# Kernel optimization log

Measured on AMD Instinct MI355X. Metric: run time of the kernel, lower is better.

## Reference

```python
import jax, jax.numpy as jnp
import numpy as np

N = 100000
IN_DIM = 128
OUT_DIM = 128
HEADS = 4
C = OUT_DIM // HEADS  # per-head channels = 32
E = 1600000
EPS = 1e-5
NEG_SLOPE = 0.2


def setup_inputs() -> dict:
    key = jax.random.key(0)
    ks = jax.random.split(key, 10)
    prev = jax.random.normal(ks[0], (N, OUT_DIM), dtype=jnp.float32)
    x = jax.random.normal(ks[1], (N, IN_DIM), dtype=jnp.float32)
    edge_index = jax.random.randint(ks[2], (2, E), 0, N, dtype=jnp.int32)
    # GATConv parameters (glorot-ish scale)
    W = jax.random.normal(ks[3], (IN_DIM, HEADS * C), dtype=jnp.float32) * (1.0 / np.sqrt(IN_DIM))
    att_src = jax.random.normal(ks[4], (HEADS, C), dtype=jnp.float32) * (1.0 / np.sqrt(C))
    att_dst = jax.random.normal(ks[5], (HEADS, C), dtype=jnp.float32) * (1.0 / np.sqrt(C))
    bias = jnp.zeros((HEADS * C,), dtype=jnp.float32)
    # BatchNorm1d affine params
    gamma = jnp.ones((OUT_DIM,), dtype=jnp.float32)
    beta = jnp.zeros((OUT_DIM,), dtype=jnp.float32)
    return {"prev": prev, "x": x, "edge_index": edge_index, "W": W,
            "att_src": att_src, "att_dst": att_dst, "bias": bias,
            "gamma": gamma, "beta": beta}


def reference(prev, x, edge_index, W, att_src, att_dst, bias, gamma, beta):
    # --- GATConv (PyG defaults: add_self_loops=True, concat=True, neg_slope=0.2) ---
    n = x.shape[0]
    # add self loops
    loops = jnp.arange(n, dtype=edge_index.dtype)
    src = jnp.concatenate([edge_index[0], loops])  # [E+N] message source j
    dst = jnp.concatenate([edge_index[1], loops])  # [E+N] message target i

    h = (x @ W).reshape(n, HEADS, C)               # [N,H,C]
    a_src = jnp.einsum('nhc,hc->nh', h, att_src)   # [N,H]
    a_dst = jnp.einsum('nhc,hc->nh', h, att_dst)   # [N,H]

    alpha = a_src[src] + a_dst[dst]                # [E',H]
    alpha = jax.nn.leaky_relu(alpha, NEG_SLOPE)
    # segment softmax over incoming edges of each dst node
    amax = jax.ops.segment_max(alpha, dst, num_segments=n)       # [N,H]
    alpha = jnp.exp(alpha - amax[dst])
    asum = jax.ops.segment_sum(alpha, dst, num_segments=n)       # [N,H]
    alpha = alpha / asum[dst]

    msg = h[src] * alpha[:, :, None]                              # [E',H,C]
    out = jax.ops.segment_sum(msg, dst, num_segments=n)          # [N,H,C]
    out = out.reshape(n, HEADS * C) + bias                       # concat heads + bias

    # --- residual + BatchNorm1d (training-mode batch stats) + activation ---
    y = prev + out
    mean = jnp.mean(y, axis=0)
    var = jnp.mean(jnp.square(y - mean), axis=0)  # biased variance (torch BN)
    y = gamma * (y - mean) * jax.lax.rsqrt(var + EPS) + beta
    return jax.nn.relu(y)
```

## Files before the change

### kernel.cpp

```cpp
#include <hip/hip_runtime.h>
#include <math.h>

#define DIM 128
#define NEG 0.2f
#define EPS 1e-5f
#define LOG2E 1.4426950408889634f

#if __has_builtin(__builtin_amdgcn_exp2f)
#define EXP2(x) __builtin_amdgcn_exp2f(x)
#else
#define EXP2(x) exp2f(x)
#endif

typedef __attribute__((ext_vector_type(8))) short short8v;
typedef __attribute__((ext_vector_type(4))) float f32x4;

static __device__ __forceinline__ float leaky(float a) { return a > 0.f ? a : NEG * a; }
static __device__ __forceinline__ float bf2f(unsigned short u) {
    return __uint_as_float(((unsigned int)u) << 16);
}
static __device__ __forceinline__ unsigned short f2bf(float f) {
    unsigned int u = __float_as_uint(f);
    unsigned int r = (u + 0x7fffu + ((u >> 16) & 1u)) >> 16;
    return (unsigned short)r;
}

__global__ __launch_bounds__(256) void k_gemm(const float* __restrict__ x,
                                              const float* __restrict__ W,
                                              const float* __restrict__ att_s,
                                              const float* __restrict__ att_d,
                                              unsigned int* __restrict__ hpk,
                                              float* __restrict__ asrc,
                                              float* __restrict__ adst, int n) {
    __shared__ __align__(16) unsigned short xs[16][136];
    const int tid = threadIdx.x;
    const int w = tid >> 6;
    const int lane = tid & 63;
    const int lm = lane & 15;
    const int lk = lane >> 4;
    short8v bfrag[2][4];
#pragma unroll
    for (int ct = 0; ct < 2; ++ct) {
        int c = w * 32 + ct * 16 + lm;
#pragma unroll
        for (int q = 0; q < 4; ++q) {
            short8v f;
#pragma unroll
            for (int j = 0; j < 8; ++j) {
                int k = q * 32 + lk * 8 + j;
                f[j] = (short)f2bf(W[k * DIM + c]);
            }
            bfrag[ct][q] = f;
        }
    }
    const float asv0 = att_s[w * 32 + lm] * LOG2E;
    const float asv1 = att_s[w * 32 + 16 + lm] * LOG2E;
    const float adv0 = att_d[w * 32 + lm] * LOG2E;
    const float adv1 = att_d[w * 32 + 16 + lm] * LOG2E;

    const int nchunk = (n + 15) >> 4;
    for (int chunk = blockIdx.x; chunk < nchunk; chunk += gridDim.x) {
        const int r0 = chunk * 16;
        {
            int row = tid >> 4;
            int c8 = (tid & 15) * 8;
            int rg = min(r0 + row, n - 1);
            const float4* xp = (const float4*)(x + (size_t)rg * DIM + c8);
            float4 v0 = xp[0], v1 = xp[1];
            short8v t;
            t[0] = (short)f2bf(v0.x); t[1] = (short)f2bf(v0.y);
            t[2] = (short)f2bf(v0.z); t[3] = (short)f2bf(v0.w);
            t[4] = (short)f2bf(v1.x); t[5] = (short)f2bf(v1.y);
            t[6] = (short)f2bf(v1.z); t[7] = (short)f2bf(v1.w);
            *(short8v*)(&xs[row][c8]) = t;
        }
        __syncthreads();
        f32x4 acc0 = {0.f, 0.f, 0.f, 0.f}, acc1 = {0.f, 0.f, 0.f, 0.f};
#pragma unroll
        for (int q = 0; q < 4; ++q) {
            short8v a = *(const short8v*)(&xs[lm][q * 32 + lk * 8]);
            acc0 = __builtin_amdgcn_mfma_f32_16x16x32_bf16(a, bfrag[0][q], acc0, 0, 0, 0);
            acc1 = __builtin_amdgcn_mfma_f32_16x16x32_bf16(a, bfrag[1][q], acc1, 0, 0, 0);
        }
        __syncthreads();
        float ps[4], qs[4];
#pragma unroll
        for (int j = 0; j < 4; ++j) {
            ps[j] = acc0[j] * asv0 + acc1[j] * asv1;
            qs[j] = acc0[j] * adv0 + acc1[j] * adv1;
        }
#pragma unroll
        for (int m = 1; m < 16; m <<= 1) {
#pragma unroll
            for (int j = 0; j < 4; ++j) {
                ps[j] += __shfl_xor(ps[j], m);
                qs[j] += __shfl_xor(qs[j], m);
            }
        }
#pragma unroll
        for (int j = 0; j < 4; ++j) {
            int r = r0 + 4 * lk + j;
            if (r < n) {
                hpk[(size_t)r * 64 + 16 * w + lm] =
                    (unsigned int)f2bf(acc0[j]) | ((unsigned int)f2bf(acc1[j]) << 16);
                if (lm == 0) {
                    asrc[r * 4 + w] = ps[j];
                    adst[r * 4 + w] = qs[j];
                }
            }
        }
    }
}

__global__ void k_init(int* __restrict__ deg, float* __restrict__ stats, int n) {
    int t = blockIdx.x * blockDim.x + threadIdx.x;
    if (t < n) deg[t] = 1;
    if (t < 256) stats[t] = 0.f;
}

__global__ __launch_bounds__(256) void k_hist(const int* __restrict__ dst,
                                              int* __restrict__ deg, int E, int n) {
    const int g = blockIdx.x & 7;
    const int gb = blockIdx.x >> 3;
    const int nblk = gridDim.x >> 3;
    const int wsz = (n + 7) >> 3;
    const int lo = g * wsz;
    const int hi = min(lo + wsz, n);
    const int step = nblk * 256;
    for (int t = gb * 256 + threadIdx.x; t < E; t += step) {
        int d = dst[t];
        if (d >= lo && d < hi) atomicAdd(&deg[d], 1);
    }
}

__global__ __launch_bounds__(256) void k_scan_part(const int* __restrict__ deg,
                                                   int* __restrict__ bsum, int n) {
    int idx = blockIdx.x * 1024 + threadIdx.x * 4;
    int4 v = {0, 0, 0, 0};
    if (idx + 3 < n) v = *(const int4*)(deg + idx);
    else {
        if (idx + 0 < n) v.x = deg[idx + 0];
        if (idx + 1 < n) v.y = deg[idx + 1];
        if (idx + 2 < n) v.z = deg[idx + 2];
    }
    int s = v.x + v.y + v.z + v.w;
#pragma unroll
    for (int m = 1; m < 64; m <<= 1) s += __shfl_xor(s, m);
    __shared__ int ws[4];
    if ((threadIdx.x & 63) == 0) ws[threadIdx.x >> 6] = s;
    __syncthreads();
    if (threadIdx.x == 0) bsum[blockIdx.x] = ws[0] + ws[1] + ws[2] + ws[3];
}

__global__ __launch_bounds__(256) void k_scan_tops(int* __restrict__ bsum, int B) {
    __shared__ int lds[256];
    int t = threadIdx.x;
    int v = (t < B) ? bsum[t] : 0;
    lds[t] = v;
    __syncthreads();
    int acc = v;
    for (int ofs = 1; ofs < 256; ofs <<= 1) {
        int u = (t >= ofs) ? lds[t - ofs] : 0;
        __syncthreads();
        acc += u;
        lds[t] = acc;
        __syncthreads();
    }
    if (t < B) bsum[t] = acc - v;
}

__global__ __launch_bounds__(256) void k_scan_add(const int* __restrict__ deg,
                                                  const int* __restrict__ bsum,
                                                  int* __restrict__ row_start,
                                                  int* __restrict__ cursor, int n, int total) {
    int t = threadIdx.x;
    int idx = blockIdx.x * 1024 + t * 4;
    int4 v = {0, 0, 0, 0};
    if (idx + 3 < n) v = *(const int4*)(deg + idx);
    else {
        if (idx + 0 < n) v.x = deg[idx + 0];
        if (idx + 1 < n) v.y = deg[idx + 1];
        if (idx + 2 < n) v.z = deg[idx + 2];
    }
    int s = v.x + v.y + v.z + v.w;
    __shared__ int lds[256];
    lds[t] = s;
    __syncthreads();
    int acc = s;
    for (int ofs = 1; ofs < 256; ofs <<= 1) {
        int u = (t >= ofs) ? lds[t - ofs] : 0;
        __syncthreads();
        acc += u;
        lds[t] = acc;
        __syncthreads();
    }
    int excl = bsum[blockIdx.x] + acc - s;
    int4 rs;
    rs.x = excl;
    rs.y = rs.x + v.x;
    rs.z = rs.y + v.y;
    rs.w = rs.z + v.z;
    if (idx + 3 < n) {
        *(int4*)(row_start + idx) = rs;
        *(int4*)(cursor + idx) = rs;
    } else {
        if (idx + 0 < n) { row_start[idx + 0] = rs.x; cursor[idx + 0] = rs.x; }
        if (idx + 1 < n) { row_start[idx + 1] = rs.y; cursor[idx + 1] = rs.y; }
        if (idx + 2 < n) { row_start[idx + 2] = rs.z; cursor[idx + 2] = rs.z; }
    }
    if (blockIdx.x == 0 && t == 0) row_start[n] = total;
}

__global__ __launch_bounds__(256) void k_scatter(const int* __restrict__ src,
                                                 const int* __restrict__ dst,
                                                 const float4* __restrict__ asrc4,
                                                 const float4* __restrict__ adst4,
                                                 int* __restrict__ cursor,
                                                 int* __restrict__ csr,
                                                 uint2* __restrict__ pw,
                                                 int E, int n) {
    const int g = blockIdx.x & 7;
    const int gb = blockIdx.x >> 3;
    const int nblk = gridDim.x >> 3;
    const int wsz = (n + 7) >> 3;
    const int lo = g * wsz;
    const int hi = min(lo + wsz, n);
    const int total = E + n;
    const int step = nblk * 256;
    for (int t = gb * 256 + threadIdx.x; t < total; t += step) {
        int d = (t < E) ? dst[t] : (t - E);
        if (d >= lo && d < hi) {
            int sv = (t < E) ? src[t] : d;
            float4 a = asrc4[sv];
            float4 b = adst4[d];
            float p0 = EXP2(leaky(a.x + b.x));
            float p1 = EXP2(leaky(a.y + b.y));
            float p2 = EXP2(leaky(a.z + b.z));
            float p3 = EXP2(leaky(a.w + b.w));
            int slot = atomicAdd(&cursor[d], 1);
            csr[slot] = sv;
            uint2 o;
            o.x = (unsigned int)f2bf(p0) | ((unsigned int)f2bf(p1) << 16);
            o.y = (unsigned int)f2bf(p2) | ((unsigned int)f2bf(p3) << 16);
            pw[slot] = o;
        }
    }
}

__global__ __launch_bounds__(256) void k_agg(const unsigned int* __restrict__ hw,
                                             const unsigned short* __restrict__ pwh,
                                             const int* __restrict__ row_start,
                                             const int* __restrict__ csr,
                                             const float* __restrict__ prev,
                                             const float* __restrict__ bias,
                                             float* __restrict__ ypre,
                                             float* __restrict__ stats, int n) {
    const int lane = threadIdx.x & 63;
    const int hd = lane >> 4;
    const int ch = 32 * hd + (lane & 15);
    int wave = blockIdx.x * 4 + (threadIdx.x >> 6);
    int nw = gridDim.x * 4;
    const float bb0 = bias[ch], bb1 = bias[ch + 16];
    float bsum0 = 0.f, bsq0 = 0.f, bsum1 = 0.f, bsq1 = 0.f;
    for (int i0 = wave; i0 < n; i0 += nw) {
        int i = __builtin_amdgcn_readfirstlane(i0);
        int e0 = row_start[i], e1 = row_start[i + 1];
        float s = 0.f, acc0 = 0.f, acc1 = 0.f;
        for (int e = e0; e < e1; e += 16) {
            int j[16];
            float p[16];
            unsigned int hp[16];
#pragma unroll
            for (int r = 0; r < 16; ++r) {
                int ec = min(e + r, e1 - 1);
                j[r] = csr[ec];
                p[r] = bf2f(pwh[ec * 4 + hd]);
            }
#pragma unroll
            for (int r = 0; r < 16; ++r) hp[r] = hw[(size_t)j[r] * 64 + lane];
#pragma unroll
            for (int r = 0; r < 16; ++r) {
                float pp = (e + r < e1) ? p[r] : 0.f;
                s += pp;
                acc0 = fmaf(pp, __uint_as_float(hp[r] << 16), acc0);
                acc1 = fmaf(pp, __uint_as_float(hp[r] & 0xffff0000u), acc1);
            }
        }
        float rs = 1.0f / s;
        size_t base = (size_t)i * DIM;
        float o0 = fmaf(acc0, rs, bb0 + prev[base + ch]);
        float o1 = fmaf(acc1, rs, bb1 + prev[base + ch + 16]);
        ypre[base + ch] = o0;
        ypre[base + ch + 16] = o1;
        bsum0 += o0; bsq0 = fmaf(o0, o0, bsq0);
        bsum1 += o1; bsq1 = fmaf(o1, o1, bsq1);
    }
    __shared__ float red[4][256];
    red[0][threadIdx.x] = bsum0;
    red[1][threadIdx.x] = bsq0;
    red[2][threadIdx.x] = bsum1;
    red[3][threadIdx.x] = bsq1;
    __syncthreads();
    if (threadIdx.x < 64) {
        int t = threadIdx.x;
        int c = 32 * (t >> 4) + (t & 15);
        float v0 = red[0][t] + red[0][t + 64] + red[0][t + 128] + red[0][t + 192];
        float v1 = red[1][t] + red[1][t + 64] + red[1][t + 128] + red[1][t + 192];
        float v2 = red[2][t] + red[2][t + 64] + red[2][t + 128] + red[2][t + 192];
        float v3 = red[3][t] + red[3][t + 64] + red[3][t + 128] + red[3][t + 192];
        atomicAdd(&stats[c], v0);
        atomicAdd(&stats[c + 16], v2);
        atomicAdd(&stats[128 + c], v1);
        atomicAdd(&stats[128 + c + 16], v3);
    }
}

__global__ void k_bnfin(const float* __restrict__ stats, const float* __restrict__ gamma,
                        const float* __restrict__ beta, float* __restrict__ AB, int n) {
    int c = threadIdx.x;
    float fn = (float)n;
    float mean = stats[c] / fn;
    float var = stats[128 + c] / fn - mean * mean;
    float a = gamma[c] * rsqrtf(var + EPS);
    AB[c] = a;
    AB[128 + c] = beta[c] - mean * a;
}

__global__ __launch_bounds__(256) void k_final(float* __restrict__ y,
                                               const float* __restrict__ AB, int total4) {
    int t0 = blockIdx.x * blockDim.x + threadIdx.x;
    int stride = gridDim.x * blockDim.x;
    for (int t = t0; t < total4; t += stride) {
        float4 v = ((float4*)y)[t];
        int c0 = (t * 4) & 127;
        v.x = fmaf(v.x, AB[c0 + 0], AB[128 + c0 + 0]);
        v.y = fmaf(v.y, AB[c0 + 1], AB[128 + c0 + 1]);
        v.z = fmaf(v.z, AB[c0 + 2], AB[128 + c0 + 2]);
        v.w = fmaf(v.w, AB[c0 + 3], AB[128 + c0 + 3]);
        v.x = v.x > 0.f ? v.x : 0.f;
        v.y = v.y > 0.f ? v.y : 0.f;
        v.z = v.z > 0.f ? v.z : 0.f;
        v.w = v.w > 0.f ? v.w : 0.f;
        ((float4*)y)[t] = v;
    }
}

extern "C" void kernel_launch(void* const* d_in, const int* in_sizes, int n_in,
                              void* d_out, int out_size, void* d_ws, size_t ws_size,
                              hipStream_t stream) {
    const float* prev  = (const float*)d_in[0];
    const float* x     = (const float*)d_in[1];
    const int*   ei    = (const int*)d_in[2];
    const float* W     = (const float*)d_in[3];
    const float* att_s = (const float*)d_in[4];
    const float* att_d = (const float*)d_in[5];
    const float* bias  = (const float*)d_in[6];
    const float* gamma = (const float*)d_in[7];
    const float* beta  = (const float*)d_in[8];
    const int n = in_sizes[0] / DIM;
    const int E = in_sizes[2] / 2;
    const int* src = ei;
    const int* dst = ei + E;

    char* p = (char*)d_ws;
    auto alloc = [&](size_t bytes) {
        void* q = (void*)p;
        p += (bytes + 255) & ~(size_t)255;
        return q;
    };
    unsigned int* hpk = (unsigned int*)alloc((size_t)n * 64 * 4);
    float* asrc      = (float*)alloc((size_t)n * 4 * 4);
    float* adst      = (float*)alloc((size_t)n * 4 * 4);
    int*   deg       = (int*)alloc((size_t)(n + 1) * 4);
    int*   row_start = (int*)alloc((size_t)(n + 1) * 4);
    int*   cursor    = (int*)alloc((size_t)(n + 1) * 4);
    int*   csr       = (int*)alloc((size_t)(E + n + 16) * 4);
    uint2* pw        = (uint2*)alloc((size_t)(E + n + 16) * 8);
    int*   bsum      = (int*)alloc(1024 * 4);
    float* stats     = (float*)alloc(256 * 4);
    float* AB        = (float*)alloc(256 * 4);
    float* yout      = (float*)d_out;

    int B = (n + 1023) / 1024;
    k_init<<<dim3((n + 255) / 256), dim3(256), 0, stream>>>(deg, stats, n);
    k_gemm<<<dim3(1024), dim3(256), 0, stream>>>(x, W, att_s, att_d, hpk, asrc, adst, n);
    k_hist<<<dim3(2048), dim3(256), 0, stream>>>(dst, deg, E, n);
    k_scan_part<<<dim3(B), dim3(256), 0, stream>>>(deg, bsum, n);
    k_scan_tops<<<dim3(1), dim3(256), 0, stream>>>(bsum, B);
    k_scan_add<<<dim3(B), dim3(256), 0, stream>>>(deg, bsum, row_start, cursor, n, E + n);
    k_scatter<<<dim3(2048), dim3(256), 0, stream>>>(src, dst, (const float4*)asrc,
                                                    (const float4*)adst, cursor, csr, pw, E, n);
    k_agg<<<dim3(2048), dim3(256), 0, stream>>>(hpk, (const unsigned short*)pw, row_start,
                                                csr, prev, bias, yout, stats, n);
    k_bnfin<<<dim3(1), dim3(128), 0, stream>>>(stats, gamma, beta, AB, n);
    int total4 = n * DIM / 4;
    k_final<<<dim3(2048), dim3(256), 0, stream>>>(yout, AB, total4);
}
```

Measured before the change: 312.2 us.

## Store pre-BN output as packed bf16 and remap agg waves to node ranges

The aggregation kernel now writes its pre-normalization output as packed bf16 pairs into a workspace buffer, and a new final kernel reads it, applies the BN affine transform and ReLU, and writes fp32. The aim is to cut the bytes of the intermediate write and read. Agg waves are also regrouped so that groups of blocks (blockIdx & 7) cover contiguous node ranges, likely to improve cache locality across XCDs. The packed path is used only when the workspace is large enough. It adds bf16 rounding of the pre-BN values, which is an accuracy risk.

Result: faster. 298.2 us (-4.5%).

```diff
diff --git a/kernel.cpp b/kernel.cpp
--- a/kernel.cpp
+++ b/kernel.cpp
@@ -247,6 +247,7 @@
     }
 }
 
+template <bool PACKED>
 __global__ __launch_bounds__(256) void k_agg(const unsigned int* __restrict__ hw,
                                              const unsigned short* __restrict__ pwh,
                                              const int* __restrict__ row_start,
@@ -254,15 +255,22 @@
                                              const float* __restrict__ prev,
                                              const float* __restrict__ bias,
                                              float* __restrict__ ypre,
+                                             unsigned int* __restrict__ ypb,
                                              float* __restrict__ stats, int n) {
     const int lane = threadIdx.x & 63;
     const int hd = lane >> 4;
     const int ch = 32 * hd + (lane & 15);
-    int wave = blockIdx.x * 4 + (threadIdx.x >> 6);
-    int nw = gridDim.x * 4;
+    const int g = blockIdx.x & 7;
+    const int gb = blockIdx.x >> 3;
+    const int nblk = gridDim.x >> 3;
+    const int wsz = (n + 7) >> 3;
+    const int lo = g * wsz;
+    const int hi = min(lo + wsz, n);
+    const int wig = gb * 4 + (threadIdx.x >> 6);
+    const int nwg = nblk * 4;
     const float bb0 = bias[ch], bb1 = bias[ch + 16];
     float bsum0 = 0.f, bsq0 = 0.f, bsum1 = 0.f, bsq1 = 0.f;
-    for (int i0 = wave; i0 < n; i0 += nw) {
+    for (int i0 = lo + wig; i0 < hi; i0 += nwg) {
         int i = __builtin_amdgcn_readfirstlane(i0);
         int e0 = row_start[i], e1 = row_start[i + 1];
         float s = 0.f, acc0 = 0.f, acc1 = 0.f;
@@ -290,8 +298,13 @@
         size_t base = (size_t)i * DIM;
         float o0 = fmaf(acc0, rs, bb0 + prev[base + ch]);
         float o1 = fmaf(acc1, rs, bb1 + prev[base + ch + 16]);
-        ypre[base + ch] = o0;
-        ypre[base + ch + 16] = o1;
+        if (PACKED) {
+            ypb[(size_t)i * 64 + lane] =
+                (unsigned int)f2bf(o0) | ((unsigned int)f2bf(o1) << 16);
+        } else {
+            ypre[base + ch] = o0;
+            ypre[base + ch + 16] = o1;
+        }
         bsum0 += o0; bsq0 = fmaf(o0, o0, bsq0);
         bsum1 += o1; bsq1 = fmaf(o1, o1, bsq1);
     }
@@ -326,6 +339,25 @@
     AB[128 + c] = beta[c] - mean * a;
 }
 
+__global__ __launch_bounds__(256) void k_final_pk(const unsigned int* __restrict__ ypb,
+                                                  const float* __restrict__ AB,
+                                                  float* __restrict__ yout, int totalw) {
+    int t0 = blockIdx.x * blockDim.x + threadIdx.x;
+    int stride = gridDim.x * blockDim.x;
+    for (int t = t0; t < totalw; t += stride) {
+        unsigned int wv = ypb[t];
+        int u = t & 63;
+        int row = t >> 6;
+        int c = 32 * (u >> 4) + (u & 15);
+        float o0 = bf2f((unsigned short)(wv & 0xffffu));
+        float o1 = bf2f((unsigned short)(wv >> 16));
+        float r0 = fmaf(o0, AB[c], AB[128 + c]);
+        float r1 = fmaf(o1, AB[c + 16], AB[128 + c + 16]);
+        yout[(size_t)row * DIM + c] = r0 > 0.f ? r0 : 0.f;
+        yout[(size_t)row * DIM + c + 16] = r1 > 0.f ? r1 : 0.f;
+    }
+}
+
 __global__ __launch_bounds__(256) void k_final(float* __restrict__ y,
                                                const float* __restrict__ AB, int total4) {
     int t0 = blockIdx.x * blockDim.x + threadIdx.x;
@@ -379,6 +411,8 @@
     int*   bsum      = (int*)alloc(1024 * 4);
     float* stats     = (float*)alloc(256 * 4);
     float* AB        = (float*)alloc(256 * 4);
+    unsigned int* ypb = (unsigned int*)alloc((size_t)n * 64 * 4);
+    const bool packed = ((size_t)(p - (char*)d_ws) <= ws_size);
     float* yout      = (float*)d_out;
 
     int B = (n + 1023) / 1024;
@@ -390,9 +424,15 @@
     k_scan_add<<<dim3(B), dim3(256), 0, stream>>>(deg, bsum, row_start, cursor, n, E + n);
     k_scatter<<<dim3(2048), dim3(256), 0, stream>>>(src, dst, (const float4*)asrc,
                                                     (const float4*)adst, cursor, csr, pw, E, n);
-    k_agg<<<dim3(2048), dim3(256), 0, stream>>>(hpk, (const unsigned short*)pw, row_start,
-                                                csr, prev, bias, yout, stats, n);
-    k_bnfin<<<dim3(1), dim3(128), 0, stream>>>(stats, gamma, beta, AB, n);
-    int total4 = n * DIM / 4;
-    k_final<<<dim3(2048), dim3(256), 0, stream>>>(yout, AB, total4);
-}
+    if (packed) {
+        k_agg<true><<<dim3(2048), dim3(256), 0, stream>>>(
+            hpk, (const unsigned short*)pw, row_start, csr, prev, bias, yout, ypb, stats, n);
+        k_bnfin<<<dim3(1), dim3(128), 0, stream>>>(stats, gamma, beta, AB, n);
+        k_final_pk<<<dim3(2048), dim3(256), 0, stream>>>(ypb, AB, yout, n * 64);
+    } else {
+        k_agg<false><<<dim3(2048), dim3(256), 0, stream>>>(
+            hpk, (const unsigned short*)pw, row_start, csr, prev, bias, yout, ypb, stats, n);
+        k_bnfin<<<dim3(1), dim3(128), 0, stream>>>(stats, gamma, beta, AB, n);
+        k_final<<<dim3(2048), dim3(256), 0, stream>>>(yout, AB, n * DIM / 4);
+    }
+}
```
